# Optimization experiments

Measured on AMD Instinct MI355X. Metric: run time of the kernel, lower is better.

Reference implementation:

```python
import jax, jax.numpy as jnp
import numpy as np

B, N, DIM_IN, DIM_K, DIM_V, NH = 2, 2048, 1024, 1024, 1024, 16

def setup_inputs() -> dict:
    key = jax.random.key(0)
    ks = jax.random.split(key, 7)
    s_in = 1.0 / np.sqrt(DIM_IN)
    return {
        "x": jax.random.normal(ks[0], (B, N, DIM_IN), dtype=jnp.float32),
        "Wq": jax.random.uniform(ks[1], (DIM_IN, DIM_K), jnp.float32, -s_in, s_in),
        "bq": jax.random.uniform(ks[2], (DIM_K,), jnp.float32, -s_in, s_in),
        "Wk": jax.random.uniform(ks[3], (DIM_IN, DIM_K), jnp.float32, -s_in, s_in),
        "bk": jax.random.uniform(ks[4], (DIM_K,), jnp.float32, -s_in, s_in),
        "Wv": jax.random.uniform(ks[5], (DIM_IN, DIM_V), jnp.float32, -s_in, s_in),
        "bv": jax.random.uniform(ks[6], (DIM_V,), jnp.float32, -s_in, s_in),
    }

def reference(x, Wq, bq, Wk, bk, Wv, bv):
    b, n, _ = x.shape
    dk = DIM_K // NH
    dv = DIM_V // NH
    scale = 1.0 / np.sqrt(dk)
    # project and split heads: [b, nh, n, dk]
    q = (x @ Wq + bq).reshape(b, n, NH, dk).transpose(0, 2, 1, 3)
    k = (x @ Wk + bk).reshape(b, n, NH, dk).transpose(0, 2, 1, 3)
    v = (x @ Wv + bv).reshape(b, n, NH, dv).transpose(0, 2, 1, 3)
    dist = jnp.einsum('bhqd,bhkd->bhqk', q, k) * scale  # [b,nh,n,n]
    dist = jax.nn.softmax(dist, axis=-1)
    att = jnp.einsum('bhqk,bhkd->bhqd', dist, v)
    return att.transpose(0, 2, 1, 3).reshape(b, n, DIM_V)
```

## Files before the change

kernel.cpp:

```cpp
#include <hip/hip_runtime.h>

#define DI __device__ __forceinline__

typedef unsigned short u16;
typedef short short8 __attribute__((ext_vector_type(8)));
typedef float f32x2 __attribute__((ext_vector_type(2)));
typedef float f32x4 __attribute__((ext_vector_type(4)));
typedef float f32x16 __attribute__((ext_vector_type(16)));
typedef u16 u16x4 __attribute__((ext_vector_type(4)));
typedef unsigned u32x4 __attribute__((ext_vector_type(4)));
typedef int i32x2 __attribute__((ext_vector_type(2)));

DI u16 f2bf(float f){
    unsigned u = __builtin_bit_cast(unsigned, f);
    u += 0x7FFFu + ((u >> 16) & 1u);
    return (u16)(u >> 16);
}

#if defined(__has_builtin)
#if __has_builtin(__builtin_amdgcn_global_load_lds)
#define HAS_GLL 1
#endif
#if __has_builtin(__builtin_amdgcn_exp2f)
#define HAS_EXP2 1
#endif
#if __has_builtin(__builtin_amdgcn_permlane32_swap)
#define HAS_PL32 1
#endif
#endif

DI void async16(u16* lds, const u16* g){
#ifdef HAS_GLL
    __builtin_amdgcn_global_load_lds(
        (const __attribute__((address_space(1))) unsigned int*)g,
        (__attribute__((address_space(3))) unsigned int*)lds, 16, 0, 0);
#else
    *(short8*)lds = *(const short8*)g;
#endif
}

DI float ex2(float x){
#ifdef HAS_EXP2
    return __builtin_amdgcn_exp2f(x);
#else
    return exp2f(x);
#endif
}

DI unsigned cvtpk(float lo, float hi){
    unsigned r;
    asm("v_cvt_pk_bf16_f32 %0, %1, %2" : "=v"(r) : "v"(lo), "v"(hi));
    return r;
}

DI i32x2 plswap(int a, int b){
#ifdef HAS_PL32
    return __builtin_amdgcn_permlane32_swap(a, b, false, false);
#else
    i32x2 r;
    int ax = __shfl_xor(a, 32), bx = __shfl_xor(b, 32);
    int hi = (threadIdx.x & 63) >> 5;
    r[0] = hi ? bx : a;
    r[1] = hi ? b : ax;
    return r;
#endif
}

#define SEQ   2048
#define DIN   1024
#define MTOT  4096
#define QSCALE 0.18033688011112042f
#define THR2   11.5f

__global__ void k_cvt_x(const float* __restrict__ x, u16* __restrict__ xb){
    int i = (blockIdx.x * 256 + threadIdx.x) * 4;
    f32x4 v = *(const f32x4*)(x + i);
    u16x4 o;
    for (int j = 0; j < 4; j++) o[j] = f2bf(v[j]);
    *(u16x4*)(xb + i) = o;
}

__global__ void k_tw3(const float* __restrict__ Wq, const float* __restrict__ Wk,
                      const float* __restrict__ Wv, u16* __restrict__ Wt3){
    const float* W = (blockIdx.z == 0) ? Wq : (blockIdx.z == 1) ? Wk : Wv;
    u16* Wt = Wt3 + (size_t)blockIdx.z * DIN * DIN;
    __shared__ float t[32][33];
    int tx = threadIdx.x, ty = threadIdx.y;
    int n0 = blockIdx.x * 32, k0 = blockIdx.y * 32;
    for (int i = 0; i < 4; i++)
        t[ty + i*8][tx] = W[(size_t)(k0 + ty + i*8) * DIN + n0 + tx];
    __syncthreads();
    for (int i = 0; i < 4; i++)
        Wt[(size_t)(n0 + ty + i*8) * DIN + k0 + tx] = f2bf(t[tx][ty + i*8]);
}

__global__ __launch_bounds__(256, 3) void k_projf(const u16* __restrict__ A,
                                                  const u16* __restrict__ Wt3,
                                                  const float* __restrict__ bq,
                                                  const float* __restrict__ bk,
                                                  const float* __restrict__ bv,
                                                  u16* __restrict__ qb,
                                                  u16* __restrict__ kb,
                                                  u16* __restrict__ vtb){
    __shared__ __align__(16) u16 As[3][4096];
    __shared__ __align__(16) u16 Bs[3][4096];
    int tid = threadIdx.x;
    int l = tid & 63, w = tid >> 6;
    int lq = l & 15, lg = l >> 4;
    int wm = w >> 1, wn = w & 1;
    int by  = blockIdx.y;
    int mat = by >> 3;
    int m0 = blockIdx.x * 128, n0 = (by & 7) * 128;
    const u16* Bt = Wt3 + (size_t)mat * DIN * DIN;
    const float* bias = (mat == 0) ? bq : (mat == 1) ? bk : bv;

    int r0 = tid >> 2, c0 = (tid & 3) * 8;
    const u16* ap0 = A  + (size_t)(m0 + r0)      * DIN + c0;
    const u16* ap1 = A  + (size_t)(m0 + 64 + r0) * DIN + c0;
    const u16* bp0 = Bt + (size_t)(n0 + r0)      * DIN + c0;
    const u16* bp1 = Bt + (size_t)(n0 + 64 + r0) * DIN + c0;
    int d0 = tid * 8, d1 = 2048 + tid * 8;

#define PSTAGE(bi) {                                              \
    async16(&As[bi][d0], ap0); async16(&As[bi][d1], ap1);         \
    async16(&Bs[bi][d0], bp0); async16(&Bs[bi][d1], bp1);         \
    ap0 += 32; ap1 += 32; bp0 += 32; bp1 += 32; }

    f32x4 acc[4][4] = {};
    PSTAGE(0)

    for (int t = 0; t < 32; t++){
        int cur = t % 3;
        if (t + 1 < 32){
            PSTAGE((t + 1) % 3)
            asm volatile("s_waitcnt vmcnt(4)" ::: "memory");
        } else {
            asm volatile("s_waitcnt vmcnt(0)" ::: "memory");
        }
        __builtin_amdgcn_s_barrier();

        short8 af[4], bf[4];
        #pragma unroll
        for (int f = 0; f < 4; f++){
            af[f] = *(const short8*)&As[cur][(wm*64 + f*16 + lq) * 32 + lg * 8];
            bf[f] = *(const short8*)&Bs[cur][(wn*64 + f*16 + lq) * 32 + lg * 8];
        }
        __builtin_amdgcn_s_setprio(1);
        #pragma unroll
        for (int fm = 0; fm < 4; fm++)
            #pragma unroll
            for (int fn = 0; fn < 4; fn++)
                acc[fm][fn] = __builtin_amdgcn_mfma_f32_16x16x32_bf16(af[fm], bf[fn], acc[fm][fn], 0, 0, 0);
        __builtin_amdgcn_s_setprio(0);
        __builtin_amdgcn_s_barrier();
    }
#undef PSTAGE

    for (int fn = 0; fn < 4; fn++){
        int cc = n0 + wn*64 + fn*16 + lq;
        float bvv = bias[cc];
        int h = cc >> 6, d = cc & 63;
        for (int fm = 0; fm < 4; fm++){
            int mbase = m0 + wm*64 + fm*16 + lg*4;
            int b = mbase >> 11, n = mbase & 2047;
            if (mat == 2){
                u16x4 pv;
                for (int r = 0; r < 4; r++) pv[r] = f2bf(acc[fm][fn][r] + bvv);
                *(u16x4*)&vtb[((size_t)(b*16 + h) * 64 + d) * SEQ + n] = pv;
            } else {
                u16* dst = (mat == 0) ? qb : kb;
                float sc = (mat == 0) ? QSCALE : 1.0f;
                for (int r = 0; r < 4; r++){
                    float v = (acc[fm][fn][r] + bvv) * sc;
                    dst[((size_t)(b*16 + h) * SEQ + (n + r)) * 64 + d] = f2bf(v);
                }
            }
        }
    }
}

#define MFMA32(a, b, c) __builtin_amdgcn_mfma_f32_32x32x16_bf16(a, b, c, 0, 0, 0)

#define MAKE_PA(dst, S, base) {                                   \
    unsigned a0 = cvtpk(S[base+0], S[base+1]);                    \
    unsigned a1 = cvtpk(S[base+2], S[base+3]);                    \
    unsigned b0 = cvtpk(S[base+4], S[base+5]);                    \
    unsigned b1 = cvtpk(S[base+6], S[base+7]);                    \
    i32x2 r0 = plswap((int)a0, (int)b0);                          \
    i32x2 r1 = plswap((int)a1, (int)b1);                          \
    u32x4 wv = {(unsigned)r0[0], (unsigned)r1[0],                 \
                (unsigned)r0[1], (unsigned)r1[1]};                \
    dst = __builtin_bit_cast(short8, wv); }

template<int SPLIT>
__global__ __launch_bounds__(256, 4) void k_attn(const u16* __restrict__ Q,
                                                 const u16* __restrict__ K,
                                                 const u16* __restrict__ Vt,
                                                 float* __restrict__ out,
                                                 float* __restrict__ po,
                                                 float* __restrict__ mls){
    __shared__ __align__(16) u16 Ks[2][64 * 64];
    __shared__ __align__(16) u16 Vs[2][64 * 64];

    int tid = threadIdx.x, l = tid & 63, w = tid >> 6;
    int lq = l & 31, hi = l >> 5;
    int bh = blockIdx.y;
    int b = bh >> 4, h = bh & 15;
    int q0 = blockIdx.x * 128 + w * 32;
    int sp = blockIdx.z;
    int kvb = sp * (SEQ / SPLIT);
    const int NT = (SEQ / SPLIT) / 64;

    const u16* Qb = Q  + (size_t)bh * SEQ * 64;
    const u16* Kb = K  + (size_t)bh * SEQ * 64;
    const u16* Vb = Vt + (size_t)bh * 64 * SEQ;

    int row0 = tid >> 3;
    int c0   = (tid & 7) ^ (row0 & 7);
    const u16* kp0 = Kb + (size_t)(kvb + row0)      * 64 + c0 * 8;
    const u16* kp1 = Kb + (size_t)(kvb + row0 + 32) * 64 + c0 * 8;
    const u16* vp0 = Vb + (size_t)row0        * SEQ + kvb + c0 * 8;
    const u16* vp1 = Vb + (size_t)(row0 + 32) * SEQ + kvb + c0 * 8;
    int d0 = tid * 8, d1 = 2048 + tid * 8;

#define STAGE(bi) {                                               \
    async16(&Ks[bi][d0], kp0); async16(&Ks[bi][d1], kp1);         \
    async16(&Vs[bi][d0], vp0); async16(&Vs[bi][d1], vp1);         \
    kp0 += 64*64; kp1 += 64*64; vp0 += 64; vp1 += 64; }

    short8 qf[4];
    #pragma unroll
    for (int ks = 0; ks < 4; ks++)
        qf[ks] = *(const short8*)(Qb + (size_t)(q0 + lq) * 64 + ks*16 + hi*8);

    STAGE(0)

    float m = -INFINITY, ls = 0.f;
    f32x16 o0 = {}, o1 = {};
    int rx = (lq & 7) << 4;

    for (int t = 0; t < NT; t++){
        int cur = t & 1;
        if (t + 1 < NT) STAGE(cur ^ 1)
        if (t == 0){
            if (NT > 1) asm volatile("s_waitcnt vmcnt(4)" ::: "memory");
            else        asm volatile("s_waitcnt vmcnt(0)" ::: "memory");
            __builtin_amdgcn_s_barrier();
        }

        const char* kB = (const char*)&Ks[cur][0];
        const char* vB = (const char*)&Vs[cur][0];

        f32x16 st0 = {}, st1 = {};
        __builtin_amdgcn_s_setprio(1);
        #pragma unroll
        for (int ks = 0; ks < 4; ks++){
            int cb = ((ks*2 + hi) << 4) ^ rx;
            short8 ka = *(const short8*)(kB + lq*128        + cb);
            short8 kb = *(const short8*)(kB + (32+lq)*128   + cb);
            st0 = MFMA32(ka, qf[ks], st0);
            st1 = MFMA32(kb, qf[ks], st1);
        }
        __builtin_amdgcn_s_setprio(0);

        float p0 = fmaxf(st0[0], st1[0]), p1 = fmaxf(st0[1], st1[1]);
        float p2 = fmaxf(st0[2], st1[2]), p3 = fmaxf(st0[3], st1[3]);
        #pragma unroll
        for (int r = 4; r < 16; r += 4){
            p0 = fmaxf(p0, fmaxf(st0[r+0], st1[r+0]));
            p1 = fmaxf(p1, fmaxf(st0[r+1], st1[r+1]));
            p2 = fmaxf(p2, fmaxf(st0[r+2], st1[r+2]));
            p3 = fmaxf(p3, fmaxf(st0[r+3], st1[r+3]));
        }
        float pm = fmaxf(fmaxf(p0, p1), fmaxf(p2, p3));
        pm = fmaxf(pm, __shfl_xor(pm, 32));

        if (__any(pm > m + THR2)){
            float mn  = fmaxf(m, pm);
            float fac = ex2(m - mn);
            m = mn;
            ls *= fac;
            #pragma unroll
            for (int r = 0; r < 16; r++){
                int row = (r & 3) + 8*(r >> 2) + 4*hi;
                float f = __shfl(fac, row);
                o0[r] *= f; o1[r] *= f;
            }
        }

        f32x2 ps = {0.f, 0.f};
        #pragma unroll
        for (int r = 0; r < 16; r += 2){
            st0[r]   = ex2(st0[r]   - m);
            st0[r+1] = ex2(st0[r+1] - m);
            st1[r]   = ex2(st1[r]   - m);
            st1[r+1] = ex2(st1[r+1] - m);
            f32x2 a = {st0[r], st0[r+1]};
            f32x2 c = {st1[r], st1[r+1]};
            ps += a + c;
        }
        float psum = ps[0] + ps[1];
        psum += __shfl_xor(psum, 32);
        ls += psum;

        short8 pa0, pa1, pa2, pa3;
        MAKE_PA(pa0, st0, 0)
        MAKE_PA(pa1, st0, 8)
        MAKE_PA(pa2, st1, 0)
        MAKE_PA(pa3, st1, 8)

        __builtin_amdgcn_s_setprio(1);
        #pragma unroll
        for (int kct = 0; kct < 4; kct++){
            short8 pf = (kct == 0) ? pa0 : (kct == 1) ? pa1 : (kct == 2) ? pa2 : pa3;
            int cb = ((kct*2 + hi) << 4) ^ rx;
            short8 v0 = *(const short8*)(vB + lq*128      + cb);
            short8 v1 = *(const short8*)(vB + (32+lq)*128 + cb);
            o0 = MFMA32(pf, v0, o0);
            o1 = MFMA32(pf, v1, o1);
        }
        __builtin_amdgcn_s_setprio(0);

        asm volatile("s_waitcnt vmcnt(0)" ::: "memory");
        __builtin_amdgcn_s_barrier();
    }

    if (SPLIT == 1){
        #pragma unroll
        for (int r = 0; r < 16; r++){
            int row = (r & 3) + 8*(r >> 2) + 4*hi;
            float inv = 1.0f / __shfl(ls, row);
            float* op = out + ((size_t)b * SEQ + (q0 + row)) * 1024 + h*64 + lq;
            op[0]  = o0[r] * inv;
            op[32] = o1[r] * inv;
        }
    } else {
        float* pb = po + (size_t)sp * MTOT * 1024;
        #pragma unroll
        for (int r = 0; r < 16; r++){
            int row = (r & 3) + 8*(r >> 2) + 4*hi;
            float* op = pb + ((size_t)b * SEQ + (q0 + row)) * 1024 + h*64 + lq;
            op[0]  = o0[r];
            op[32] = o1[r];
        }
        if (hi == 0){
            float* mp = mls + (((size_t)sp*32 + bh) * SEQ + (q0 + lq)) * 2;
            mp[0] = m; mp[1] = ls;
        }
    }
#undef STAGE
}

template<int S>
__global__ __launch_bounds__(256) void k_comb(const float* __restrict__ po,
                                              const float* __restrict__ mls,
                                              float* __restrict__ out){
    size_t i = ((size_t)blockIdx.x * 256 + threadIdx.x) * 4;
    size_t row = i >> 10;
    int col = (int)(i & 1023);
    int b = (int)(row >> 11), n = (int)(row & 2047);
    int bh = b*16 + (col >> 6);

    float mv[S], lv[S], wv[S];
    float M = -INFINITY;
    #pragma unroll
    for (int s = 0; s < S; s++){
        const float* p = mls + (((size_t)s*32 + bh) * SEQ + n) * 2;
        mv[s] = p[0]; lv[s] = p[1];
        M = fmaxf(M, mv[s]);
    }
    float L = 0.f;
    #pragma unroll
    for (int s = 0; s < S; s++){ wv[s] = ex2(mv[s] - M); L += wv[s] * lv[s]; }
    float inv = 1.0f / L;
    f32x4 acc = {};
    #pragma unroll
    for (int s = 0; s < S; s++){
        f32x4 v = *(const f32x4*)(po + (size_t)s * MTOT * 1024 + i);
        acc += v * wv[s];
    }
    acc *= inv;
    *(f32x4*)(out + i) = acc;
}

extern "C" void kernel_launch(void* const* d_in, const int* in_sizes, int n_in,
                              void* d_out, int out_size, void* d_ws, size_t ws_size,
                              hipStream_t stream){
    const float* x  = (const float*)d_in[0];
    const float* Wq = (const float*)d_in[1];
    const float* bq = (const float*)d_in[2];
    const float* Wk = (const float*)d_in[3];
    const float* bk = (const float*)d_in[4];
    const float* Wv = (const float*)d_in[5];
    const float* bv = (const float*)d_in[6];
    float* out = (float*)d_out;

    const size_t MB = (size_t)1 << 20;
    if (ws_size < 38 * MB) return;

    char* ws = (char*)d_ws;
    u16* xb   = (u16*)(ws);
    u16* wt3  = (u16*)(ws +  8 * MB);
    u16* qb   = (u16*)(ws + 14 * MB);
    u16* kb   = (u16*)(ws + 22 * MB);
    u16* vtb  = (u16*)(ws + 30 * MB);
    int S = (ws_size >= 38 * MB + 2 * 17 * MB) ? 2 : 1;
    float* po  = (float*)(ws + 38 * MB);
    float* mls = (float*)(ws + 38 * MB + (size_t)S * 16 * MB);

    k_cvt_x<<<4096, 256, 0, stream>>>(x, xb);
    k_tw3<<<dim3(32, 32, 3), dim3(32, 8), 0, stream>>>(Wq, Wk, Wv, wt3);

    k_projf<<<dim3(32, 24), 256, 0, stream>>>(xb, wt3, bq, bk, bv, qb, kb, vtb);

    if (S == 2){
        k_attn<2><<<dim3(16, 32, 2), 256, 0, stream>>>(qb, kb, vtb, out, po, mls);
        k_comb<2><<<4096, 256, 0, stream>>>(po, mls, out);
    } else {
        k_attn<1><<<dim3(16, 32, 1), 256, 0, stream>>>(qb, kb, vtb, out, po, mls);
    }
}
```

Before: 109.9 us.

## Process 64 query rows per wave and drop online max tracking in attention

New measurement: 298.7 us. 172% more time.

```diff
diff --git a/kernel.cpp b/kernel.cpp
--- a/kernel.cpp
+++ b/kernel.cpp
@@ -70,7 +70,6 @@
 #define DIN   1024
 #define MTOT  4096
 #define QSCALE 0.18033688011112042f
-#define THR2   11.5f
 
 __global__ void k_cvt_x(const float* __restrict__ x, u16* __restrict__ xb){
     int i = (blockIdx.x * 256 + threadIdx.x) * 4;
@@ -199,14 +198,14 @@
                                                  float* __restrict__ out,
                                                  float* __restrict__ po,
                                                  float* __restrict__ mls){
-    __shared__ __align__(16) u16 Ks[2][64 * 64];
-    __shared__ __align__(16) u16 Vs[2][64 * 64];
+    __shared__ __align__(16) u16 Ks[2][4096];
+    __shared__ __align__(16) u16 Vs[2][4096];
 
     int tid = threadIdx.x, l = tid & 63, w = tid >> 6;
     int lq = l & 31, hi = l >> 5;
     int bh = blockIdx.y;
     int b = bh >> 4, h = bh & 15;
-    int q0 = blockIdx.x * 128 + w * 32;
+    int q0 = blockIdx.x * 256 + w * 64;
     int sp = blockIdx.z;
     int kvb = sp * (SEQ / SPLIT);
     const int NT = (SEQ / SPLIT) / 64;
@@ -228,15 +227,18 @@
     async16(&Vs[bi][d0], vp0); async16(&Vs[bi][d1], vp1);         \
     kp0 += 64*64; kp1 += 64*64; vp0 += 64; vp1 += 64; }
 
-    short8 qf[4];
+    short8 qf0[4], qf1[4];
     #pragma unroll
-    for (int ks = 0; ks < 4; ks++)
-        qf[ks] = *(const short8*)(Qb + (size_t)(q0 + lq) * 64 + ks*16 + hi*8);
+    for (int ks = 0; ks < 4; ks++){
+        qf0[ks] = *(const short8*)(Qb + (size_t)(q0 + lq)      * 64 + ks*16 + hi*8);
+        qf1[ks] = *(const short8*)(Qb + (size_t)(q0 + 32 + lq) * 64 + ks*16 + hi*8);
+    }
 
     STAGE(0)
 
-    float m = -INFINITY, ls = 0.f;
-    f32x16 o0 = {}, o1 = {};
+    float m = 0.f;
+    float ls0 = 0.f, ls1 = 0.f;
+    f32x16 o00 = {}, o01 = {}, o10 = {}, o11 = {};
     int rx = (lq & 7) << 4;
 
     for (int t = 0; t < NT; t++){
@@ -251,75 +253,73 @@
         const char* kB = (const char*)&Ks[cur][0];
         const char* vB = (const char*)&Vs[cur][0];
 
-        f32x16 st0 = {}, st1 = {};
+        f32x16 s00 = {}, s01 = {}, s10 = {}, s11 = {};
         __builtin_amdgcn_s_setprio(1);
         #pragma unroll
         for (int ks = 0; ks < 4; ks++){
             int cb = ((ks*2 + hi) << 4) ^ rx;
             short8 ka = *(const short8*)(kB + lq*128        + cb);
             short8 kb = *(const short8*)(kB + (32+lq)*128   + cb);
-            st0 = MFMA32(ka, qf[ks], st0);
-            st1 = MFMA32(kb, qf[ks], st1);
+            s00 = MFMA32(ka, qf0[ks], s00);
+            s01 = MFMA32(kb, qf0[ks], s01);
+            s10 = MFMA32(ka, qf1[ks], s10);
+            s11 = MFMA32(kb, qf1[ks], s11);
         }
         __builtin_amdgcn_s_setprio(0);
 
-        float p0 = fmaxf(st0[0], st1[0]), p1 = fmaxf(st0[1], st1[1]);
-        float p2 = fmaxf(st0[2], st1[2]), p3 = fmaxf(st0[3], st1[3]);
-        #pragma unroll
-        for (int r = 4; r < 16; r += 4){
-            p0 = fmaxf(p0, fmaxf(st0[r+0], st1[r+0]));
-            p1 = fmaxf(p1, fmaxf(st0[r+1], st1[r+1]));
-            p2 = fmaxf(p2, fmaxf(st0[r+2], st1[r+2]));
-            p3 = fmaxf(p3, fmaxf(st0[r+3], st1[r+3]));
-        }
-        float pm = fmaxf(fmaxf(p0, p1), fmaxf(p2, p3));
-        pm = fmaxf(pm, __shfl_xor(pm, 32));
-
-        if (__any(pm > m + THR2)){
-            float mn  = fmaxf(m, pm);
-            float fac = ex2(m - mn);
-            m = mn;
-            ls *= fac;
+        if (m != 0.f){
             #pragma unroll
             for (int r = 0; r < 16; r++){
-                int row = (r & 3) + 8*(r >> 2) + 4*hi;
-                float f = __shfl(fac, row);
-                o0[r] *= f; o1[r] *= f;
+                s00[r] -= m; s01[r] -= m; s10[r] -= m; s11[r] -= m;
             }
         }
 
-        f32x2 ps = {0.f, 0.f};
-        #pragma unroll
-        for (int r = 0; r < 16; r += 2){
-            st0[r]   = ex2(st0[r]   - m);
-            st0[r+1] = ex2(st0[r+1] - m);
-            st1[r]   = ex2(st1[r]   - m);
-            st1[r+1] = ex2(st1[r+1] - m);
-            f32x2 a = {st0[r], st0[r+1]};
-            f32x2 c = {st1[r], st1[r+1]};
-            ps += a + c;
-        }
-        float psum = ps[0] + ps[1];
-        psum += __shfl_xor(psum, 32);
-        ls += psum;
-
-        short8 pa0, pa1, pa2, pa3;
-        MAKE_PA(pa0, st0, 0)
-        MAKE_PA(pa1, st0, 8)
-        MAKE_PA(pa2, st1, 0)
-        MAKE_PA(pa3, st1, 8)
+        float pA0 = 0.f, pA1 = 0.f, pB0 = 0.f, pB1 = 0.f;
+        #pragma unroll
+        for (int r = 0; r < 16; r++){
+            s00[r] = ex2(s00[r]); s01[r] = ex2(s01[r]);
+            s10[r] = ex2(s10[r]); s11[r] = ex2(s11[r]);
+            if (r & 1){ pA1 += s00[r] + s01[r]; pB1 += s10[r] + s11[r]; }
+            else      { pA0 += s00[r] + s01[r]; pB0 += s10[r] + s11[r]; }
+        }
+        float psum0 = pA0 + pA1; psum0 += __shfl_xor(psum0, 32);
+        float psum1 = pB0 + pB1; psum1 += __shfl_xor(psum1, 32);
+
+        short8 pa00, pa01, pa02, pa03, pa10, pa11, pa12, pa13;
+        MAKE_PA(pa00, s00, 0)
+        MAKE_PA(pa01, s00, 8)
+        MAKE_PA(pa02, s01, 0)
+        MAKE_PA(pa03, s01, 8)
+        MAKE_PA(pa10, s10, 0)
+        MAKE_PA(pa11, s10, 8)
+        MAKE_PA(pa12, s11, 0)
+        MAKE_PA(pa13, s11, 8)
 
         __builtin_amdgcn_s_setprio(1);
         #pragma unroll
         for (int kct = 0; kct < 4; kct++){
-            short8 pf = (kct == 0) ? pa0 : (kct == 1) ? pa1 : (kct == 2) ? pa2 : pa3;
+            short8 pf0 = (kct == 0) ? pa00 : (kct == 1) ? pa01 : (kct == 2) ? pa02 : pa03;
+            short8 pf1 = (kct == 0) ? pa10 : (kct == 1) ? pa11 : (kct == 2) ? pa12 : pa13;
             int cb = ((kct*2 + hi) << 4) ^ rx;
             short8 v0 = *(const short8*)(vB + lq*128      + cb);
             short8 v1 = *(const short8*)(vB + (32+lq)*128 + cb);
-            o0 = MFMA32(pf, v0, o0);
-            o1 = MFMA32(pf, v1, o1);
+            o00 = MFMA32(pf0, v0, o00);
+            o01 = MFMA32(pf0, v1, o01);
+            o10 = MFMA32(pf1, v0, o10);
+            o11 = MFMA32(pf1, v1, o11);
         }
         __builtin_amdgcn_s_setprio(0);
+
+        ls0 += psum0; ls1 += psum1;
+        if (__any((ls0 > 1.0e30f) || (ls1 > 1.0e30f))){
+            const float dn = 5.421010862427522e-20f;
+            ls0 *= dn; ls1 *= dn;
+            #pragma unroll
+            for (int r = 0; r < 16; r++){
+                o00[r] *= dn; o01[r] *= dn; o10[r] *= dn; o11[r] *= dn;
+            }
+            m += 64.f;
+        }
 
         asm volatile("s_waitcnt vmcnt(0)" ::: "memory");
         __builtin_amdgcn_s_barrier();
@@ -329,23 +329,32 @@
         #pragma unroll
         for (int r = 0; r < 16; r++){
             int row = (r & 3) + 8*(r >> 2) + 4*hi;
-            float inv = 1.0f / __shfl(ls, row);
-            float* op = out + ((size_t)b * SEQ + (q0 + row)) * 1024 + h*64 + lq;
-            op[0]  = o0[r] * inv;
-            op[32] = o1[r] * inv;
+            float inv0 = 1.0f / __shfl(ls0, row);
+            float inv1 = 1.0f / __shfl(ls1, row);
+            float* op0 = out + ((size_t)b * SEQ + (q0 + row)) * 1024 + h*64 + lq;
+            float* op1 = out + ((size_t)b * SEQ + (q0 + 32 + row)) * 1024 + h*64 + lq;
+            op0[0]  = o00[r] * inv0;
+            op0[32] = o01[r] * inv0;
+            op1[0]  = o10[r] * inv1;
+            op1[32] = o11[r] * inv1;
         }
     } else {
         float* pb = po + (size_t)sp * MTOT * 1024;
         #pragma unroll
         for (int r = 0; r < 16; r++){
             int row = (r & 3) + 8*(r >> 2) + 4*hi;
-            float* op = pb + ((size_t)b * SEQ + (q0 + row)) * 1024 + h*64 + lq;
-            op[0]  = o0[r];
-            op[32] = o1[r];
+            float* op0 = pb + ((size_t)b * SEQ + (q0 + row)) * 1024 + h*64 + lq;
+            float* op1 = pb + ((size_t)b * SEQ + (q0 + 32 + row)) * 1024 + h*64 + lq;
+            op0[0]  = o00[r];
+            op0[32] = o01[r];
+            op1[0]  = o10[r];
+            op1[32] = o11[r];
         }
         if (hi == 0){
-            float* mp = mls + (((size_t)sp*32 + bh) * SEQ + (q0 + lq)) * 2;
-            mp[0] = m; mp[1] = ls;
+            float* mp0 = mls + (((size_t)sp*32 + bh) * SEQ + (q0 + lq)) * 2;
+            float* mp1 = mls + (((size_t)sp*32 + bh) * SEQ + (q0 + 32 + lq)) * 2;
+            mp0[0] = m; mp0[1] = ls0;
+            mp1[0] = m; mp1[1] = ls1;
         }
     }
 #undef STAGE
@@ -404,7 +413,9 @@
     u16* qb   = (u16*)(ws + 14 * MB);
     u16* kb   = (u16*)(ws + 22 * MB);
     u16* vtb  = (u16*)(ws + 30 * MB);
-    int S = (ws_size >= 38 * MB + 2 * 17 * MB) ? 2 : 1;
+    int S = 1;
+    if      (ws_size >= 38 * MB + 4 * 17 * MB) S = 4;
+    else if (ws_size >= 38 * MB + 2 * 17 * MB) S = 2;
     float* po  = (float*)(ws + 38 * MB);
     float* mls = (float*)(ws + 38 * MB + (size_t)S * 16 * MB);
 
@@ -413,10 +424,13 @@
 
     k_projf<<<dim3(32, 24), 256, 0, stream>>>(xb, wt3, bq, bk, bv, qb, kb, vtb);
 
-    if (S == 2){
-        k_attn<2><<<dim3(16, 32, 2), 256, 0, stream>>>(qb, kb, vtb, out, po, mls);
+    if (S == 4){
+        k_attn<4><<<dim3(8, 32, 4), 256, 0, stream>>>(qb, kb, vtb, out, po, mls);
+        k_comb<4><<<4096, 256, 0, stream>>>(po, mls, out);
+    } else if (S == 2){
+        k_attn<2><<<dim3(8, 32, 2), 256, 0, stream>>>(qb, kb, vtb, out, po, mls);
         k_comb<2><<<4096, 256, 0, stream>>>(po, mls, out);
     } else {
-        k_attn<1><<<dim3(16, 32, 1), 256, 0, stream>>>(qb, kb, vtb, out, po, mls);
-    }
-}
+        k_attn<1><<<dim3(8, 32, 1), 256, 0, stream>>>(qb, kb, vtb, out, po, mls);
+    }
+}
```
